# Kernel tuning notes

Measured on AMD Instinct MI355X. Metric: run time of the kernel, lower is better.

## Reference

```python
import jax, jax.numpy as jnp
import numpy as np

B, S, H, R = 2, 1024, 512, 64


def setup_inputs() -> dict:
    key = jax.random.key(0)
    k1, k2, k3 = jax.random.split(key, 3)
    hidden_states = jax.random.normal(k1, (B, S, H), dtype=jnp.float32)
    # all_indices is the row-major cartesian product (seq_idx, hidden_idx),
    # as required by the final .view(batch, seq_len, hidden_size) in the module.
    si = jnp.repeat(jnp.arange(S, dtype=jnp.int64), H)
    hi = jnp.tile(jnp.arange(H, dtype=jnp.int64), S)
    all_indices = jnp.stack([si, hi], axis=1)  # [S*H, 2]
    W_seq = jax.random.normal(k2, (R, H), dtype=jnp.float32) * (1.0 / np.sqrt(H))
    hidden_embeddings = jax.random.normal(k3, (H, R), dtype=jnp.float32) * 0.02
    cp_weight = jnp.ones((1, R), dtype=jnp.float32)  # CP buffer, all ones
    return {
        "hidden_states": hidden_states,
        "all_indices": all_indices,
        "W_seq": W_seq,
        "hidden_embeddings": hidden_embeddings,
        "cp_weight": cp_weight,
    }


def reference(hidden_states, all_indices, W_seq, hidden_embeddings, cp_weight):
    b, s, h = hidden_states.shape
    # seq_mode_factor: Linear(hidden_size -> rank), no bias
    seq_emb = jnp.einsum("bsh,rh->bsr", hidden_states, W_seq)  # [B,S,R]
    si = all_indices[:, 0]  # [N]
    hi = all_indices[:, 1]  # [N]
    # Fold the (all-ones) CP weight into the hidden-mode factor, then
    # gather + hadamard + rank reduction in one fused expression.
    hid_fac = hidden_embeddings * cp_weight[0][None, :]  # [H,R]
    out = jnp.einsum("bnr,nr->bn", seq_emb[:, si, :], hid_fac[hi, :])  # [B,N]
    n = all_indices.shape[0]
    return out.reshape(b, s, n // s)  # [B,S,H], out_units=1 squeezed
```

## Files before the change

kernel.cpp:

```cpp
#include <hip/hip_runtime.h>


typedef __bf16 bf16x8 __attribute__((ext_vector_type(8)));
typedef float f32x4 __attribute__((ext_vector_type(4)));

__global__ __launch_bounds__(256) void cp_K(
    const float* __restrict__ W,
    const float* __restrict__ he,
    const float* __restrict__ cp,
    __bf16* __restrict__ KT)
{
    __shared__ float s_he[2][64];
    const int t = threadIdx.x;
    const int h0 = blockIdx.x * 2;
    if (t < 128) {
        const int hh = t >> 6, r = t & 63;
        s_he[hh][r] = he[(h0 + hh) * 64 + r] * cp[r];
    }
    __syncthreads();

    float a00 = 0.f, a01 = 0.f, a10 = 0.f, a11 = 0.f;
#pragma unroll 8
    for (int r = 0; r < 64; ++r) {
        const float w0 = W[r * 512 + t];
        const float w1 = W[r * 512 + t + 256];
        const float e0 = s_he[0][r];
        const float e1 = s_he[1][r];
        a00 += e0 * w0; a01 += e0 * w1;
        a10 += e1 * w0; a11 += e1 * w1;
    }
    KT[(size_t)h0 * 512 + t]             = (__bf16)a00;
    KT[(size_t)h0 * 512 + t + 256]       = (__bf16)a01;
    KT[(size_t)(h0 + 1) * 512 + t]       = (__bf16)a10;
    KT[(size_t)(h0 + 1) * 512 + t + 256] = (__bf16)a11;
}

__global__ __launch_bounds__(256) void cp_gemm_mfma(
    const float* __restrict__ hs,
    const __bf16* __restrict__ KT,
    float* __restrict__ out)
{
    const int t = threadIdx.x;
    const int w = t >> 6;
    const int L = t & 63;
    const int mq = L & 15;
    const int kq = L >> 4;

    const int bx = blockIdx.x;
    const int idx = (bx & 7) * 128 + (bx >> 3);
    const int mt = idx >> 4, nt = idx & 15;

    const int m0 = mt * 32 + (w >> 1) * 16;
    const int n0 = nt * 32 + (w & 1) * 16;

    const float*  aRow = hs + (size_t)(m0 + mq) * 512 + kq * 8;
    const __bf16* bRow = KT + (size_t)(n0 + mq) * 512 + kq * 8;

    f32x4 acc = {0.f, 0.f, 0.f, 0.f};
#pragma unroll 4
    for (int ks = 0; ks < 16; ++ks) {
        const float4 f0 = *(const float4*)(aRow + ks * 32);
        const float4 f1 = *(const float4*)(aRow + ks * 32 + 4);
        const bf16x8 b  = *(const bf16x8*)(bRow + ks * 32);
        bf16x8 a;
        a[0] = (__bf16)f0.x; a[1] = (__bf16)f0.y; a[2] = (__bf16)f0.z; a[3] = (__bf16)f0.w;
        a[4] = (__bf16)f1.x; a[5] = (__bf16)f1.y; a[6] = (__bf16)f1.z; a[7] = (__bf16)f1.w;
        acc = __builtin_amdgcn_mfma_f32_16x16x32_bf16(a, b, acc, 0, 0, 0);
    }

    float* op = out + (size_t)(m0 + kq * 4) * 512 + n0 + mq;
    op[0]        = acc[0];
    op[512]      = acc[1];
    op[2 * 512]  = acc[2];
    op[3 * 512]  = acc[3];
}

extern "C" void kernel_launch(void* const* d_in, const int* in_sizes, int n_in,
                              void* d_out, int out_size, void* d_ws, size_t ws_size,
                              hipStream_t stream) {
    const float* hs = (const float*)d_in[0];
    const float* W  = (const float*)d_in[2];
    const float* he = (const float*)d_in[3];
    const float* cp = (const float*)d_in[4];
    float* out = (float*)d_out;
    __bf16* KT = (__bf16*)d_ws;

    cp_K<<<dim3(256), dim3(256), 0, stream>>>(W, he, cp, KT);
    cp_gemm_mfma<<<dim3(1024), dim3(256), 0, stream>>>(hs, KT, out);
}
```

Before: 89.58 us.

## Pre-convert hidden states to bf16 in prep kernel and enlarge GEMM tile

The prep kernel now also converts hidden_states (2048x512 fp32) to bf16 in workspace, and each K block computes four rows instead of two. The MFMA GEMM now reads bf16 A directly. Each wave computes a 16x32 output tile, reusing its A fragment across two MFMAs, which halves the block count. The aim is fewer redundant fp32 A loads and converts in the GEMM, at the cost of an extra full pass writing and re-reading hidden states through workspace.

Result: faster. 80.65 us (-10.0%).

```diff
diff --git a/kernel.cpp b/kernel.cpp
--- a/kernel.cpp
+++ b/kernel.cpp
@@ -1,42 +1,67 @@
 #include <hip/hip_runtime.h>
 
 
+typedef __bf16 bf16x4 __attribute__((ext_vector_type(4)));
 typedef __bf16 bf16x8 __attribute__((ext_vector_type(8)));
 typedef float f32x4 __attribute__((ext_vector_type(4)));
 
-__global__ __launch_bounds__(256) void cp_K(
+__global__ __launch_bounds__(256) void cp_prep(
+    const float* __restrict__ hs,
     const float* __restrict__ W,
     const float* __restrict__ he,
     const float* __restrict__ cp,
+    __bf16* __restrict__ hsb,
     __bf16* __restrict__ KT)
 {
-    __shared__ float s_he[2][64];
     const int t = threadIdx.x;
-    const int h0 = blockIdx.x * 2;
-    if (t < 128) {
-        const int hh = t >> 6, r = t & 63;
-        s_he[hh][r] = he[(h0 + hh) * 64 + r] * cp[r];
+    const int b = blockIdx.x;
+
+    if (b < 256) {
+        const float4* src = (const float4*)hs + (size_t)b * 1024;
+        bf16x4* dst = (bf16x4*)hsb + (size_t)b * 1024;
+#pragma unroll
+        for (int i = 0; i < 4; ++i) {
+            const float4 v = src[t + i * 256];
+            bf16x4 o;
+            o[0] = (__bf16)v.x; o[1] = (__bf16)v.y;
+            o[2] = (__bf16)v.z; o[3] = (__bf16)v.w;
+            dst[t + i * 256] = o;
+        }
+        return;
+    }
+
+    __shared__ float s_he[4][64];
+    const int h0 = (b - 256) * 4;
+    if (t < 64) {
+        const float4 v = ((const float4*)(he + (size_t)h0 * 64))[t];
+        const float4 c = ((const float4*)cp)[t & 15];
+        float* d = &s_he[t >> 4][4 * (t & 15)];
+        d[0] = v.x * c.x; d[1] = v.y * c.y; d[2] = v.z * c.z; d[3] = v.w * c.w;
     }
     __syncthreads();
 
-    float a00 = 0.f, a01 = 0.f, a10 = 0.f, a11 = 0.f;
+    float a0[4] = {0.f, 0.f, 0.f, 0.f};
+    float a1[4] = {0.f, 0.f, 0.f, 0.f};
 #pragma unroll 8
     for (int r = 0; r < 64; ++r) {
         const float w0 = W[r * 512 + t];
         const float w1 = W[r * 512 + t + 256];
-        const float e0 = s_he[0][r];
-        const float e1 = s_he[1][r];
-        a00 += e0 * w0; a01 += e0 * w1;
-        a10 += e1 * w0; a11 += e1 * w1;
+#pragma unroll
+        for (int h = 0; h < 4; ++h) {
+            const float e = s_he[h][r];
+            a0[h] += e * w0;
+            a1[h] += e * w1;
+        }
     }
-    KT[(size_t)h0 * 512 + t]             = (__bf16)a00;
-    KT[(size_t)h0 * 512 + t + 256]       = (__bf16)a01;
-    KT[(size_t)(h0 + 1) * 512 + t]       = (__bf16)a10;
-    KT[(size_t)(h0 + 1) * 512 + t + 256] = (__bf16)a11;
+#pragma unroll
+    for (int h = 0; h < 4; ++h) {
+        KT[(size_t)(h0 + h) * 512 + t]       = (__bf16)a0[h];
+        KT[(size_t)(h0 + h) * 512 + t + 256] = (__bf16)a1[h];
+    }
 }
 
 __global__ __launch_bounds__(256) void cp_gemm_mfma(
-    const float* __restrict__ hs,
+    const __bf16* __restrict__ A,
     const __bf16* __restrict__ KT,
     float* __restrict__ out)
 {
@@ -47,32 +72,34 @@
     const int kq = L >> 4;
 
     const int bx = blockIdx.x;
-    const int idx = (bx & 7) * 128 + (bx >> 3);
+    const int idx = (bx & 7) * 64 + (bx >> 3);
     const int mt = idx >> 4, nt = idx & 15;
 
-    const int m0 = mt * 32 + (w >> 1) * 16;
-    const int n0 = nt * 32 + (w & 1) * 16;
+    const int m0 = mt * 64 + w * 16;
+    const int n0 = nt * 32;
 
-    const float*  aRow = hs + (size_t)(m0 + mq) * 512 + kq * 8;
-    const __bf16* bRow = KT + (size_t)(n0 + mq) * 512 + kq * 8;
+    const __bf16* aRow  = A  + (size_t)(m0 + mq) * 512 + kq * 8;
+    const __bf16* bRow0 = KT + (size_t)(n0 + mq) * 512 + kq * 8;
+    const __bf16* bRow1 = bRow0 + 16 * 512;
 
-    f32x4 acc = {0.f, 0.f, 0.f, 0.f};
+    f32x4 acc0 = {0.f, 0.f, 0.f, 0.f};
+    f32x4 acc1 = {0.f, 0.f, 0.f, 0.f};
 #pragma unroll 4
     for (int ks = 0; ks < 16; ++ks) {
-        const float4 f0 = *(const float4*)(aRow + ks * 32);
-        const float4 f1 = *(const float4*)(aRow + ks * 32 + 4);
-        const bf16x8 b  = *(const bf16x8*)(bRow + ks * 32);
-        bf16x8 a;
-        a[0] = (__bf16)f0.x; a[1] = (__bf16)f0.y; a[2] = (__bf16)f0.z; a[3] = (__bf16)f0.w;
-        a[4] = (__bf16)f1.x; a[5] = (__bf16)f1.y; a[6] = (__bf16)f1.z; a[7] = (__bf16)f1.w;
-        acc = __builtin_amdgcn_mfma_f32_16x16x32_bf16(a, b, acc, 0, 0, 0);
+        const bf16x8 a  = *(const bf16x8*)(aRow  + ks * 32);
+        const bf16x8 b0 = *(const bf16x8*)(bRow0 + ks * 32);
+        const bf16x8 b1 = *(const bf16x8*)(bRow1 + ks * 32);
+        acc0 = __builtin_amdgcn_mfma_f32_16x16x32_bf16(a, b0, acc0, 0, 0, 0);
+        acc1 = __builtin_amdgcn_mfma_f32_16x16x32_bf16(a, b1, acc1, 0, 0, 0);
     }
 
-    float* op = out + (size_t)(m0 + kq * 4) * 512 + n0 + mq;
-    op[0]        = acc[0];
-    op[512]      = acc[1];
-    op[2 * 512]  = acc[2];
-    op[3 * 512]  = acc[3];
+    float* op0 = out + (size_t)(m0 + kq * 4) * 512 + n0 + mq;
+    float* op1 = op0 + 16;
+#pragma unroll
+    for (int i = 0; i < 4; ++i) {
+        op0[i * 512] = acc0[i];
+        op1[i * 512] = acc1[i];
+    }
 }
 
 extern "C" void kernel_launch(void* const* d_in, const int* in_sizes, int n_in,
@@ -83,8 +110,10 @@
     const float* he = (const float*)d_in[3];
     const float* cp = (const float*)d_in[4];
     float* out = (float*)d_out;
-    __bf16* KT = (__bf16*)d_ws;
 
-    cp_K<<<dim3(256), dim3(256), 0, stream>>>(W, he, cp, KT);
-    cp_gemm_mfma<<<dim3(1024), dim3(256), 0, stream>>>(hs, KT, out);
+    __bf16* KT  = (__bf16*)d_ws;
+    __bf16* hsb = (__bf16*)((char*)d_ws + (512 * 1024));
+
+    cp_prep<<<dim3(384), dim3(256), 0, stream>>>(hs, W, he, cp, hsb, KT);
+    cp_gemm_mfma<<<dim3(512), dim3(256), 0, stream>>>(hsb, KT, out);
 }
```

## Fuse K-matrix precompute into GEMM kernel with per-block LDS recompute

Applied to the files above, without the earlier changes.

Removes the separate kernel that builds the combined HxH weight matrix KT in global memory. Each block now recomputes its own 32-column slice of KT with MFMA from he and W, stores it in padded shared memory, and then runs the main GEMM against that slice. The output tile grows to 64x32 per block, and each wave computes two 16x16 tiles that share the A fragment. This saves one launch and the global round trip for KT. In exchange, every one of the 512 blocks redoes the KT slice work, including strided uncoalesced loads of W that are converted to bf16 in registers, and the 33KB LDS footprint may limit occupancy.

New measurement: 78.46 us. 12.4% less time.

```diff
diff --git a/kernel.cpp b/kernel.cpp
--- a/kernel.cpp
+++ b/kernel.cpp
@@ -4,42 +4,17 @@
 typedef __bf16 bf16x8 __attribute__((ext_vector_type(8)));
 typedef float f32x4 __attribute__((ext_vector_type(4)));
 
-__global__ __launch_bounds__(256) void cp_K(
+#define KPAD 520
+
+__global__ __launch_bounds__(256) void cp_fused_v7(
+    const float* __restrict__ hs,
     const float* __restrict__ W,
     const float* __restrict__ he,
     const float* __restrict__ cp,
-    __bf16* __restrict__ KT)
-{
-    __shared__ float s_he[2][64];
-    const int t = threadIdx.x;
-    const int h0 = blockIdx.x * 2;
-    if (t < 128) {
-        const int hh = t >> 6, r = t & 63;
-        s_he[hh][r] = he[(h0 + hh) * 64 + r] * cp[r];
-    }
-    __syncthreads();
-
-    float a00 = 0.f, a01 = 0.f, a10 = 0.f, a11 = 0.f;
-#pragma unroll 8
-    for (int r = 0; r < 64; ++r) {
-        const float w0 = W[r * 512 + t];
-        const float w1 = W[r * 512 + t + 256];
-        const float e0 = s_he[0][r];
-        const float e1 = s_he[1][r];
-        a00 += e0 * w0; a01 += e0 * w1;
-        a10 += e1 * w0; a11 += e1 * w1;
-    }
-    KT[(size_t)h0 * 512 + t]             = (__bf16)a00;
-    KT[(size_t)h0 * 512 + t + 256]       = (__bf16)a01;
-    KT[(size_t)(h0 + 1) * 512 + t]       = (__bf16)a10;
-    KT[(size_t)(h0 + 1) * 512 + t + 256] = (__bf16)a11;
-}
-
-__global__ __launch_bounds__(256) void cp_gemm_mfma(
-    const float* __restrict__ hs,
-    const __bf16* __restrict__ KT,
     float* __restrict__ out)
 {
+    __shared__ __bf16 KTloc[32 * KPAD];
+
     const int t = threadIdx.x;
     const int w = t >> 6;
     const int L = t & 63;
@@ -47,32 +22,84 @@
     const int kq = L >> 4;
 
     const int bx = blockIdx.x;
-    const int idx = (bx & 7) * 128 + (bx >> 3);
+    const int idx = (bx & 7) * 64 + (bx >> 3);
     const int mt = idx >> 4, nt = idx & 15;
 
-    const int m0 = mt * 32 + (w >> 1) * 16;
-    const int n0 = nt * 32 + (w & 1) * 16;
+    const int m0 = mt * 64 + w * 16;
+    const int n0 = nt * 32;
+
+    {
+        bf16x8 af[2][2];
+#pragma unroll
+        for (int tm = 0; tm < 2; ++tm)
+#pragma unroll
+            for (int ks = 0; ks < 2; ++ks) {
+                const float* hp = he + (size_t)(n0 + tm * 16 + mq) * 64 + ks * 32 + kq * 8;
+                const float4 h0 = *(const float4*)hp;
+                const float4 h1 = *(const float4*)(hp + 4);
+                const float4 c0 = *(const float4*)(cp + ks * 32 + kq * 8);
+                const float4 c1 = *(const float4*)(cp + ks * 32 + kq * 8 + 4);
+                bf16x8 a;
+                a[0] = (__bf16)(h0.x * c0.x); a[1] = (__bf16)(h0.y * c0.y);
+                a[2] = (__bf16)(h0.z * c0.z); a[3] = (__bf16)(h0.w * c0.w);
+                a[4] = (__bf16)(h1.x * c1.x); a[5] = (__bf16)(h1.y * c1.y);
+                a[6] = (__bf16)(h1.z * c1.z); a[7] = (__bf16)(h1.w * c1.w);
+                af[tm][ks] = a;
+            }
+
+#pragma unroll
+        for (int i = 0; i < 8; ++i) {
+            const int tnG = w * 8 + i;
+            bf16x8 bf[2];
+#pragma unroll
+            for (int ks = 0; ks < 2; ++ks) {
+                const float* wp = W + (size_t)(ks * 32 + kq * 8) * 512 + tnG * 16 + mq;
+                bf16x8 b;
+#pragma unroll
+                for (int j = 0; j < 8; ++j)
+                    b[j] = (__bf16)wp[j * 512];
+                bf[ks] = b;
+            }
+#pragma unroll
+            for (int tm = 0; tm < 2; ++tm) {
+                f32x4 acc = {0.f, 0.f, 0.f, 0.f};
+                acc = __builtin_amdgcn_mfma_f32_16x16x32_bf16(af[tm][0], bf[0], acc, 0, 0, 0);
+                acc = __builtin_amdgcn_mfma_f32_16x16x32_bf16(af[tm][1], bf[1], acc, 0, 0, 0);
+                __bf16* dp = &KTloc[(tm * 16 + kq * 4) * KPAD + tnG * 16 + mq];
+#pragma unroll
+                for (int r = 0; r < 4; ++r)
+                    dp[r * KPAD] = (__bf16)acc[r];
+            }
+        }
+    }
+    __syncthreads();
 
     const float*  aRow = hs + (size_t)(m0 + mq) * 512 + kq * 8;
-    const __bf16* bRow = KT + (size_t)(n0 + mq) * 512 + kq * 8;
+    const __bf16* bR0  = &KTloc[(0  + mq) * KPAD + kq * 8];
+    const __bf16* bR1  = &KTloc[(16 + mq) * KPAD + kq * 8];
 
-    f32x4 acc = {0.f, 0.f, 0.f, 0.f};
+    f32x4 acc0 = {0.f, 0.f, 0.f, 0.f};
+    f32x4 acc1 = {0.f, 0.f, 0.f, 0.f};
 #pragma unroll 4
     for (int ks = 0; ks < 16; ++ks) {
         const float4 f0 = *(const float4*)(aRow + ks * 32);
         const float4 f1 = *(const float4*)(aRow + ks * 32 + 4);
-        const bf16x8 b  = *(const bf16x8*)(bRow + ks * 32);
+        const bf16x8 b0 = *(const bf16x8*)(bR0 + ks * 32);
+        const bf16x8 b1 = *(const bf16x8*)(bR1 + ks * 32);
         bf16x8 a;
         a[0] = (__bf16)f0.x; a[1] = (__bf16)f0.y; a[2] = (__bf16)f0.z; a[3] = (__bf16)f0.w;
         a[4] = (__bf16)f1.x; a[5] = (__bf16)f1.y; a[6] = (__bf16)f1.z; a[7] = (__bf16)f1.w;
-        acc = __builtin_amdgcn_mfma_f32_16x16x32_bf16(a, b, acc, 0, 0, 0);
+        acc0 = __builtin_amdgcn_mfma_f32_16x16x32_bf16(a, b0, acc0, 0, 0, 0);
+        acc1 = __builtin_amdgcn_mfma_f32_16x16x32_bf16(a, b1, acc1, 0, 0, 0);
     }
 
-    float* op = out + (size_t)(m0 + kq * 4) * 512 + n0 + mq;
-    op[0]        = acc[0];
-    op[512]      = acc[1];
-    op[2 * 512]  = acc[2];
-    op[3 * 512]  = acc[3];
+    float* op0 = out + (size_t)(m0 + kq * 4) * 512 + n0 + mq;
+    float* op1 = op0 + 16;
+#pragma unroll
+    for (int i = 0; i < 4; ++i) {
+        op0[i * 512] = acc0[i];
+        op1[i * 512] = acc1[i];
+    }
 }
 
 extern "C" void kernel_launch(void* const* d_in, const int* in_sizes, int n_in,
@@ -83,8 +110,6 @@
     const float* he = (const float*)d_in[3];
     const float* cp = (const float*)d_in[4];
     float* out = (float*)d_out;
-    __bf16* KT = (__bf16*)d_ws;
 
-    cp_K<<<dim3(256), dim3(256), 0, stream>>>(W, he, cp, KT);
-    cp_gemm_mfma<<<dim3(1024), dim3(256), 0, stream>>>(hs, KT, out);
+    cp_fused_v7<<<dim3(512), dim3(256), 0, stream>>>(hs, W, he, cp, out);
 }
```
